# Performance work log

Hardware: AMD Instinct MI355X
Metric: run time of the kernel (lower is better)

Reference implementation:

```python
import jax, jax.numpy as jnp
import numpy as np
from math import sqrt

T_TEMP = 1.0  # softmax temperature (init arg T)
NEG_INF = -1e30  # finite stand-in for -inf; masked probs are exactly 0 after softmax


def setup_inputs() -> dict:
    key = jax.random.key(0)
    kq, kk, kv = jax.random.split(key, 3)
    B, L, H, E = 4, 2048, 16, 64
    queries = jax.random.normal(kq, (B, L, H, E), dtype=jnp.float32)
    keys = jax.random.normal(kk, (B, L, H, E), dtype=jnp.float32)
    values = jax.random.normal(kv, (B, L, H, E), dtype=jnp.float32)
    return {"queries": queries, "keys": keys, "values": values}


def reference(queries, keys, values):
    # queries: [B,L,H,E], keys: [B,S,H,E], values: [B,S,H,D]
    B, L, H, E = queries.shape
    S = keys.shape[1]
    scale = 1.0 / sqrt(E)
    # scores: [B,H,L,S]
    scores = jnp.einsum('blhe,bshe->bhls', queries, keys) * scale
    # causal mask: True above diagonal -> masked out (TriangularCausalMask)
    causal = jnp.triu(jnp.ones((L, S), dtype=bool), k=1)
    scores = jnp.where(causal, NEG_INF, scores)
    A = jax.nn.softmax(scores / T_TEMP, axis=-1)  # dropout p=0 -> identity
    V = jnp.einsum('bhls,bshd->blhd', A, values)
    return V
```

## Files before the change

### kernel.cpp

```cpp
#include <hip/hip_runtime.h>


typedef __attribute__((ext_vector_type(8))) unsigned short u16x8;
typedef __attribute__((ext_vector_type(4))) unsigned short u16x4;
typedef __attribute__((ext_vector_type(8))) __bf16 bf16x8;
typedef __attribute__((ext_vector_type(4))) float f32x4;
typedef __attribute__((ext_vector_type(16))) float f32x16;
typedef __attribute__((ext_vector_type(4))) unsigned int u32x4;

#define LOG2E 1.44269504088896340736f
#define AS1 __attribute__((address_space(1)))
#define AS3 __attribute__((address_space(3)))

static __device__ __forceinline__ unsigned short f32_bf16_rne(float x) {
    unsigned int b = __builtin_bit_cast(unsigned int, x);
    b = (b + 0x7fffu + ((b >> 16) & 1u)) >> 16;
    return (unsigned short)b;
}

static __device__ __forceinline__ unsigned int cvt_pk_bf16(float lo, float hi) {
    unsigned int r;
    asm("v_cvt_pk_bf16_f32 %0, %1, %2" : "=v"(r) : "v"(lo), "v"(hi));
    return r;
}

static __device__ __forceinline__ int swzs(int row) {
    return (row & 6) | ((row >> 3) & 1);
}
static __device__ __forceinline__ int tileIdx(int row, int col) {
    return row * 64 + (((col >> 3) ^ swzs(row)) << 3) + (col & 7);
}

__global__ __launch_bounds__(256) void prep_kernel(
    const float* __restrict__ K, const float* __restrict__ V,
    unsigned short* __restrict__ wsK, unsigned short* __restrict__ wsV)
{
    const int ROW = 1024;
    const int tid = threadIdx.x;
    const int kt  = blockIdx.x;
    const int bh  = blockIdx.y;
    const size_t tileBase = (size_t)(bh >> 4) * 2048 * ROW + (size_t)(bh & 15) * 64
                          + (size_t)(kt * 64) * ROW;
    unsigned short* kimg = wsK + (((size_t)bh * 32 + kt) << 12);
    unsigned short* vimg = wsV + (((size_t)bh * 32 + kt) << 12);

    __shared__ __align__(16) unsigned short ik[4096];
    __shared__ unsigned int sT[64 * 33];

    {
        const int key = tid & 63, ec = tid >> 6;
        const float* kr = K + tileBase + (size_t)key * ROW + ec * 16;
        #pragma unroll
        for (int i = 0; i < 4; ++i) {
            f32x4 v = *(const f32x4*)(kr + 4 * i);
            u16x4 w;
            #pragma unroll
            for (int j = 0; j < 4; ++j) w[j] = f32_bf16_rne(v[j]);
            const int e = ec * 16 + 4 * i;
            *(u16x4*)&ik[(e >> 3) * 512 + key * 8 + (e & 7)] = w;
        }
    }

    {
        const int kp = tid & 31, d0 = (tid >> 5) * 8;
        const float* v0 = V + tileBase + (size_t)(2 * kp) * ROW + d0;
        f32x4 a0 = *(const f32x4*)(v0);
        f32x4 a1 = *(const f32x4*)(v0 + 4);
        f32x4 b0 = *(const f32x4*)(v0 + ROW);
        f32x4 b1 = *(const f32x4*)(v0 + ROW + 4);
        #pragma unroll
        for (int i = 0; i < 4; ++i) {
            sT[(d0 + i) * 33 + kp]     = cvt_pk_bf16(a0[i], b0[i]);
            sT[(d0 + 4 + i) * 33 + kp] = cvt_pk_bf16(a1[i], b1[i]);
        }
    }
    __syncthreads();

    {
        const u32x4* src = (const u32x4*)ik;
        u32x4* dst = (u32x4*)kimg;
        dst[tid]       = src[tid];
        dst[256 + tid] = src[256 + tid];
    }
    {
        u32x4* vd = (u32x4*)vimg;
        u32x4 w0, w1;
        #pragma unroll
        for (int j = 0; j < 4; ++j) {
            const int unit = tid;
            const int kc8 = unit >> 6, dx = unit & 63;
            const int d = dx ^ kc8, kp = kc8 * 4 + j;
            w0[j] = sT[d * 33 + kp];
        }
        #pragma unroll
        for (int j = 0; j < 4; ++j) {
            const int unit = 256 + tid;
            const int kc8 = unit >> 6, dx = unit & 63;
            const int d = dx ^ kc8, kp = kc8 * 4 + j;
            w1[j] = sT[d * 33 + kp];
        }
        vd[tid]       = w0;
        vd[256 + tid] = w1;
    }
}

__global__ __launch_bounds__(256, 4) void fattn2_kernel(
    const float* __restrict__ Q,
    const unsigned short* __restrict__ wsK,
    const unsigned short* __restrict__ wsV,
    float* __restrict__ O)
{
    const int ROW = 1024;

    const int tid  = threadIdx.x;
    const int wave = tid >> 6;
    const int lane = tid & 63;
    const int s    = lane >> 5;
    const int n32  = lane & 31;
    const bool hi32 = (s != 0);
    const int qh = wave & 1;
    const int kh = wave >> 1;

    const int id    = blockIdx.x;
    const int qtile = 31 - (id >> 6);
    const int bh    = id & 63;
    const size_t headBase = (size_t)(bh >> 4) * 2048 * ROW + (size_t)(bh & 15) * 64;
    const int q0 = qtile * 64 + qh * 32;

    __shared__ __align__(16) unsigned short sK[2][4096];
    __shared__ __align__(16) unsigned short sV[2][4096];

    const int kBase = s * 1024 + n32 * 16 + kh * 512;
    int vbB[2];
    #pragma unroll
    for (int c = 0; c < 2; ++c)
        vbB[c] = kh * 4096 + c * 2048 + s * 1024
               + ((n32 ^ (4 * kh + 2 * c + s)) << 4);

    const float c0 = 0.125f * LOG2E;

    bf16x8 qf[4];
    {
        const float* qrow = Q + headBase + (size_t)(q0 + n32) * ROW + s * 8;
        #pragma unroll
        for (int c = 0; c < 4; ++c) {
            f32x4 v0 = *(const f32x4*)(qrow + 16 * c);
            f32x4 v1 = *(const f32x4*)(qrow + 16 * c + 4);
            u32x4 a;
            a[0] = cvt_pk_bf16(v0[0] * c0, v0[1] * c0);
            a[1] = cvt_pk_bf16(v0[2] * c0, v0[3] * c0);
            a[2] = cvt_pk_bf16(v1[0] * c0, v1[1] * c0);
            a[3] = cvt_pk_bf16(v1[2] * c0, v1[3] * c0);
            qf[c] = __builtin_bit_cast(bf16x8, a);
        }
    }

    f32x16 oacc0, oacc1;
    #pragma unroll
    for (int r = 0; r < 16; ++r) { oacc0[r] = 0.f; oacc1[r] = 0.f; }
    float l = 0.f;

    const int nT = qtile + 1;

    #define STAGE(buf, kt_)                                                    \
    do {                                                                       \
        const size_t toff = (((size_t)bh * 32 + (kt_)) << 12);                 \
        const unsigned short* kg = wsK + toff + wave * 1024 + lane * 8;        \
        const unsigned short* vg = wsV + toff + wave * 1024 + lane * 8;        \
        __builtin_amdgcn_global_load_lds((const AS1 unsigned int*)kg,          \
            (AS3 unsigned int*)&sK[buf][wave * 1024], 16, 0, 0);               \
        __builtin_amdgcn_global_load_lds((const AS1 unsigned int*)(kg + 512),  \
            (AS3 unsigned int*)&sK[buf][wave * 1024 + 512], 16, 0, 0);         \
        __builtin_amdgcn_global_load_lds((const AS1 unsigned int*)vg,          \
            (AS3 unsigned int*)&sV[buf][wave * 1024], 16, 0, 0);               \
        __builtin_amdgcn_global_load_lds((const AS1 unsigned int*)(vg + 512),  \
            (AS3 unsigned int*)&sV[buf][wave * 1024 + 512], 16, 0, 0);         \
    } while (0)

    STAGE(0, 0);

    for (int kt = 0; kt < nT; ++kt) {
        const int cur = kt & 1;

        __syncthreads();

        if (kt + 1 < nT) STAGE(cur ^ 1, kt + 1);

        if (kt == qtile && kh > qh) continue;

        const char* kb = (const char*)&sK[cur][0];
        const char* vb = (const char*)&sV[cur][0];

        f32x16 sacc;
        #pragma unroll
        for (int r = 0; r < 16; ++r) sacc[r] = 0.f;
        __builtin_amdgcn_s_setprio(1);
        #pragma unroll
        for (int c = 0; c < 4; ++c) {
            bf16x8 k0 = __builtin_bit_cast(bf16x8,
                *(const u16x8*)(kb + kBase + c * 2048));
            sacc = __builtin_amdgcn_mfma_f32_32x32x16_bf16(k0, qf[c], sacc, 0, 0, 0);
        }
        __builtin_amdgcn_s_setprio(0);

        if (kt == qtile && kh == qh) {
            #pragma unroll
            for (int r = 0; r < 16; ++r) {
                const int k0 = (r & 3) + 8 * (r >> 2) + 4 * s;
                sacc[r] = (k0 > n32) ? -1e30f : sacc[r];
            }
        }

        float la = 0.f;
        #pragma unroll
        for (int r = 0; r < 16; ++r) {
            sacc[r] = __builtin_amdgcn_exp2f(fminf(sacc[r], 80.f));
            la += sacc[r];
        }
        l += la;

        bf16x8 bp[2];
        #define XCHG(pe, cc, DST)                                              \
        do {                                                                   \
            unsigned int P0 = cvt_pk_bf16(pe[8*(cc)+0], pe[8*(cc)+1]);         \
            unsigned int P1 = cvt_pk_bf16(pe[8*(cc)+2], pe[8*(cc)+3]);         \
            unsigned int P2 = cvt_pk_bf16(pe[8*(cc)+4], pe[8*(cc)+5]);         \
            unsigned int P3 = cvt_pk_bf16(pe[8*(cc)+6], pe[8*(cc)+7]);         \
            unsigned int x0 = __shfl_xor(P0, 32, 64);                          \
            unsigned int x1 = __shfl_xor(P1, 32, 64);                          \
            unsigned int x2 = __shfl_xor(P2, 32, 64);                          \
            unsigned int x3 = __shfl_xor(P3, 32, 64);                          \
            u32x4 bw;                                                          \
            bw[0] = hi32 ? x2 : P0;                                            \
            bw[1] = hi32 ? x3 : P1;                                            \
            bw[2] = hi32 ? P2 : x0;                                            \
            bw[3] = hi32 ? P3 : x1;                                            \
            DST = __builtin_bit_cast(bf16x8, bw);                              \
        } while (0)
        XCHG(sacc, 0, bp[0]);
        XCHG(sacc, 1, bp[1]);
        #undef XCHG

        __builtin_amdgcn_s_setprio(1);
        #pragma unroll
        for (int c = 0; c < 2; ++c) {
            bf16x8 v0 = __builtin_bit_cast(bf16x8,
                *(const u16x8*)(vb + vbB[c]));
            bf16x8 v1 = __builtin_bit_cast(bf16x8,
                *(const u16x8*)(vb + vbB[c] + 512));
            oacc0 = __builtin_amdgcn_mfma_f32_32x32x16_bf16(v0, bp[c], oacc0, 0, 0, 0);
            oacc1 = __builtin_amdgcn_mfma_f32_32x32x16_bf16(v1, bp[c], oacc1, 0, 0, 0);
        }
        __builtin_amdgcn_s_setprio(0);
    }
    #undef STAGE

    l += __shfl_xor(l, 32, 64);

    __syncthreads();

    float* lbuf = (float*)&sV[0][0];
    lbuf[wave * 32 + n32] = l;
    float* tb = (float*)&sK[0][0] + qh * 2048;
    if (kh == 1) {
        #pragma unroll
        for (int rr = 0; rr < 4; ++rr) {
            f32x4 w0, w1;
            #pragma unroll
            for (int j = 0; j < 4; ++j) {
                w0[j] = oacc0[4 * rr + j];
                w1[j] = oacc1[4 * rr + j];
            }
            const int s40 = 2 * rr + s;
            const int s41 = 8 + 2 * rr + s;
            *(f32x4*)&tb[n32 * 64 + ((s40 ^ (n32 & 15)) << 2)] = w0;
            *(f32x4*)&tb[n32 * 64 + ((s41 ^ (n32 & 15)) << 2)] = w1;
        }
    }
    __syncthreads();
    if (kh == 0) {
        const float inv = 1.0f / (l + lbuf[64 + qh * 32 + n32]);
        #pragma unroll
        for (int rr = 0; rr < 4; ++rr) {
            const int s40 = 2 * rr + s;
            const int s41 = 8 + 2 * rr + s;
            float* a0 = &tb[n32 * 64 + ((s40 ^ (n32 & 15)) << 2)];
            float* a1 = &tb[n32 * 64 + ((s41 ^ (n32 & 15)) << 2)];
            f32x4 p0 = *(const f32x4*)a0;
            f32x4 p1 = *(const f32x4*)a1;
            #pragma unroll
            for (int j = 0; j < 4; ++j) {
                p0[j] = (p0[j] + oacc0[4 * rr + j]) * inv;
                p1[j] = (p1[j] + oacc1[4 * rr + j]) * inv;
            }
            *(f32x4*)a0 = p0;
            *(f32x4*)a1 = p1;
        }
        #pragma unroll
        for (int it = 0; it < 8; ++it) {
            const int row = (lane >> 2) + 16 * (it & 1);
            const int c4  = (lane & 3) + 4 * (it >> 1);
            f32x4 v = *(const f32x4*)&tb[row * 64 + ((c4 ^ (row & 15)) << 2)];
            *(f32x4*)&O[headBase + (size_t)(q0 + row) * ROW + c4 * 4] = v;
        }
    }
}

__global__ __launch_bounds__(256, 4) void fattn_kernel(
    const float* __restrict__ Q,
    const float* __restrict__ K,
    const float* __restrict__ V,
    float* __restrict__ O)
{
    const int ROW = 1024;
    const int tid  = threadIdx.x;
    const int wave = tid >> 6;
    const int lane = tid & 63;
    const int quad = lane >> 4;
    const int n16  = lane & 15;
    const int xb = blockIdx.x;
    const int bh = blockIdx.y;
    const size_t headBase = (size_t)(bh >> 4) * 2048 * ROW + (size_t)(bh & 15) * 64;

    __shared__ __align__(16) unsigned short sK[4096];
    __shared__ __align__(16) unsigned short sV[4096];
    __shared__ __align__(16) unsigned short sP[4][1024];

    int kvIdx[4];
    #pragma unroll
    for (int nb = 0; nb < 4; ++nb) {
        const int row = nb * 16 + n16;
        kvIdx[nb] = row * 64 + ((quad ^ swzs(row)) << 3);
    }
    const int pIdx = n16 * 64 + ((quad ^ swzs(n16)) << 3);
    const int kStageRow = tid >> 4;
    const int kStageCol = (tid & 15) * 4;
    const int vKey2  = (tid & 31) * 2;
    const int vDbase = (tid >> 5) * 8;
    const float c0 = 0.125f * LOG2E;

    for (int qi = 0; qi < 2; ++qi) {
        const int qtile = qi ? (31 - xb) : xb;
        const int q0 = qtile * 64 + wave * 16;
        bf16x8 qf0, qf1;
        {
            const float* qrow = Q + headBase + (size_t)(q0 + n16) * ROW + quad * 8;
            u16x8 a, b;
            #pragma unroll
            for (int i = 0; i < 8; ++i) {
                a[i] = f32_bf16_rne(qrow[i] * c0);
                b[i] = f32_bf16_rne(qrow[32 + i] * c0);
            }
            qf0 = __builtin_bit_cast(bf16x8, a);
            qf1 = __builtin_bit_cast(bf16x8, b);
        }
        f32x4 oacc[4];
        #pragma unroll
        for (int d = 0; d < 4; ++d) oacc[d] = (f32x4){0.f, 0.f, 0.f, 0.f};
        float l_r[4];
        #pragma unroll
        for (int r = 0; r < 4; ++r) l_r[r] = 0.f;
        const int nT = qtile + 1;
        f32x4 pk[4], pva[2], pvb[2];
        {
            const float* kb = K + headBase;
            const float* r0 = V + headBase + (size_t)vKey2 * ROW + vDbase;
            #pragma unroll
            for (int j = 0; j < 4; ++j)
                pk[j] = *(const f32x4*)(kb + (size_t)(j * 16 + kStageRow) * ROW + kStageCol);
            #pragma unroll
            for (int j = 0; j < 2; ++j) {
                pva[j] = *(const f32x4*)(r0 + j * 4);
                pvb[j] = *(const f32x4*)(r0 + ROW + j * 4);
            }
        }
        for (int kt = 0; kt < nT; ++kt) {
            __syncthreads();
            #pragma unroll
            for (int j = 0; j < 4; ++j) {
                u16x4 w;
                #pragma unroll
                for (int i = 0; i < 4; ++i) w[i] = f32_bf16_rne(pk[j][i]);
                *(u16x4*)&sK[tileIdx(j * 16 + kStageRow, kStageCol)] = w;
            }
            #pragma unroll
            for (int j = 0; j < 2; ++j) {
                const int d0 = vDbase + j * 4;
                #pragma unroll
                for (int i = 0; i < 4; ++i) {
                    unsigned int pkk = (unsigned int)f32_bf16_rne(pva[j][i])
                                     | ((unsigned int)f32_bf16_rne(pvb[j][i]) << 16);
                    *(unsigned int*)&sV[tileIdx(d0 + i, vKey2)] = pkk;
                }
            }
            if (kt + 1 < nT) {
                const size_t nb2 = headBase + (size_t)((kt + 1) * 64) * ROW;
                const float* kb = K + nb2;
                const float* r0 = V + nb2 + (size_t)vKey2 * ROW + vDbase;
                #pragma unroll
                for (int j = 0; j < 4; ++j)
                    pk[j] = *(const f32x4*)(kb + (size_t)(j * 16 + kStageRow) * ROW + kStageCol);
                #pragma unroll
                for (int j = 0; j < 2; ++j) {
                    pva[j] = *(const f32x4*)(r0 + j * 4);
                    pvb[j] = *(const f32x4*)(r0 + ROW + j * 4);
                }
            }
            __syncthreads();
            f32x4 sacc[4];
            #pragma unroll
            for (int nb = 0; nb < 4; ++nb) {
                bf16x8 b0 = __builtin_bit_cast(bf16x8, *(const u16x8*)&sK[kvIdx[nb]]);
                bf16x8 b1 = __builtin_bit_cast(bf16x8, *(const u16x8*)&sK[kvIdx[nb] ^ 32]);
                f32x4 ss = (f32x4){0.f, 0.f, 0.f, 0.f};
                ss = __builtin_amdgcn_mfma_f32_16x16x32_bf16(qf0, b0, ss, 0, 0, 0);
                ss = __builtin_amdgcn_mfma_f32_16x16x32_bf16(qf1, b1, ss, 0, 0, 0);
                sacc[nb] = ss;
            }
            if (kt == qtile) {
                #pragma unroll
                for (int nb = 0; nb < 4; ++nb) {
                    const int keyl = nb * 16 + n16;
                    #pragma unroll
                    for (int r = 0; r < 4; ++r) {
                        const int ql = wave * 16 + quad * 4 + r;
                        sacc[nb][r] = (keyl > ql) ? -1e30f : sacc[nb][r];
                    }
                }
            }
            #pragma unroll
            for (int r = 0; r < 4; ++r) {
                const int qrl = quad * 4 + r;
                const int pwBase = qrl * 64 + (n16 & 7);
                const int sw = swzs(qrl);
                const int hb = n16 >> 3;
                float ps = 0.f;
                #pragma unroll
                for (int nb = 0; nb < 4; ++nb) {
                    unsigned short u = f32_bf16_rne(__builtin_amdgcn_exp2f(sacc[nb][r]));
                    ps += __builtin_bit_cast(float, (unsigned int)u << 16);
                    sP[wave][pwBase + (((nb * 2 + hb) ^ sw) << 3)] = u;
                }
                l_r[r] += ps;
            }
            #pragma unroll
            for (int kh = 0; kh < 2; ++kh) {
                bf16x8 ap = __builtin_bit_cast(bf16x8,
                    *(const u16x8*)&sP[wave][pIdx ^ (kh << 5)]);
                #pragma unroll
                for (int d = 0; d < 4; ++d) {
                    bf16x8 vf = __builtin_bit_cast(bf16x8,
                        *(const u16x8*)&sV[kvIdx[d] ^ (kh << 5)]);
                    oacc[d] = __builtin_amdgcn_mfma_f32_16x16x32_bf16(ap, vf, oacc[d], 0, 0, 0);
                }
            }
        }
        float inv[4];
        #pragma unroll
        for (int r = 0; r < 4; ++r) {
            float l = l_r[r];
            #pragma unroll
            for (int off = 1; off < 16; off <<= 1)
                l += __shfl_xor(l, off, 64);
            inv[r] = 1.0f / l;
        }
        #pragma unroll
        for (int d = 0; d < 4; ++d) {
            #pragma unroll
            for (int r = 0; r < 4; ++r) {
                const int qg = q0 + quad * 4 + r;
                O[headBase + (size_t)qg * ROW + d * 16 + n16] = oacc[d][r] * inv[r];
            }
        }
    }
}

extern "C" void kernel_launch(void* const* d_in, const int* in_sizes, int n_in,
                              void* d_out, int out_size, void* d_ws, size_t ws_size,
                              hipStream_t stream) {
    const float* Q = (const float*)d_in[0];
    const float* K = (const float*)d_in[1];
    const float* V = (const float*)d_in[2];
    float* Out = (float*)d_out;

    const size_t imgElems = (size_t)64 * 32 * 4096;
    if (ws_size >= imgElems * 2 * sizeof(unsigned short)) {
        unsigned short* wsK = (unsigned short*)d_ws;
        unsigned short* wsV = wsK + imgElems;
        hipLaunchKernelGGL(prep_kernel, dim3(32, 64), dim3(256), 0, stream, K, V, wsK, wsV);
        hipLaunchKernelGGL(fattn2_kernel, dim3(2048), dim3(256), 0, stream, Q, wsK, wsV, Out);
    } else {
        hipLaunchKernelGGL(fattn_kernel, dim3(16, 64), dim3(256), 0, stream, Q, K, V, Out);
    }
}
```

Before: 191.3 us.

## Fuse K/V bf16 conversion into attention kernel, dropping separate prep pass

Removes the prep kernel that converted K and V to bf16 tile images in workspace. The attention kernel now loads fp32 K/V tiles directly into registers one tile ahead, converts them to bf16, and writes them into swizzled LDS before each step. This saves one kernel launch and the write and read-back of the workspace images. In exchange, each block re-reads and re-converts fp32 K/V, which doubles global bytes per tile and redoes the conversion many times across query tiles. It also replaces the async global-to-LDS copies with register staging, adding VGPR pressure. The old fallback kernel is deleted.

```diff
diff --git a/kernel.cpp b/kernel.cpp
--- a/kernel.cpp
+++ b/kernel.cpp
@@ -2,21 +2,12 @@
 
 
 typedef __attribute__((ext_vector_type(8))) unsigned short u16x8;
-typedef __attribute__((ext_vector_type(4))) unsigned short u16x4;
 typedef __attribute__((ext_vector_type(8))) __bf16 bf16x8;
 typedef __attribute__((ext_vector_type(4))) float f32x4;
 typedef __attribute__((ext_vector_type(16))) float f32x16;
 typedef __attribute__((ext_vector_type(4))) unsigned int u32x4;
 
 #define LOG2E 1.44269504088896340736f
-#define AS1 __attribute__((address_space(1)))
-#define AS3 __attribute__((address_space(3)))
-
-static __device__ __forceinline__ unsigned short f32_bf16_rne(float x) {
-    unsigned int b = __builtin_bit_cast(unsigned int, x);
-    b = (b + 0x7fffu + ((b >> 16) & 1u)) >> 16;
-    return (unsigned short)b;
-}
 
 static __device__ __forceinline__ unsigned int cvt_pk_bf16(float lo, float hi) {
     unsigned int r;
@@ -24,90 +15,10 @@
     return r;
 }
 
-static __device__ __forceinline__ int swzs(int row) {
-    return (row & 6) | ((row >> 3) & 1);
-}
-static __device__ __forceinline__ int tileIdx(int row, int col) {
-    return row * 64 + (((col >> 3) ^ swzs(row)) << 3) + (col & 7);
-}
-
-__global__ __launch_bounds__(256) void prep_kernel(
-    const float* __restrict__ K, const float* __restrict__ V,
-    unsigned short* __restrict__ wsK, unsigned short* __restrict__ wsV)
-{
-    const int ROW = 1024;
-    const int tid = threadIdx.x;
-    const int kt  = blockIdx.x;
-    const int bh  = blockIdx.y;
-    const size_t tileBase = (size_t)(bh >> 4) * 2048 * ROW + (size_t)(bh & 15) * 64
-                          + (size_t)(kt * 64) * ROW;
-    unsigned short* kimg = wsK + (((size_t)bh * 32 + kt) << 12);
-    unsigned short* vimg = wsV + (((size_t)bh * 32 + kt) << 12);
-
-    __shared__ __align__(16) unsigned short ik[4096];
-    __shared__ unsigned int sT[64 * 33];
-
-    {
-        const int key = tid & 63, ec = tid >> 6;
-        const float* kr = K + tileBase + (size_t)key * ROW + ec * 16;
-        #pragma unroll
-        for (int i = 0; i < 4; ++i) {
-            f32x4 v = *(const f32x4*)(kr + 4 * i);
-            u16x4 w;
-            #pragma unroll
-            for (int j = 0; j < 4; ++j) w[j] = f32_bf16_rne(v[j]);
-            const int e = ec * 16 + 4 * i;
-            *(u16x4*)&ik[(e >> 3) * 512 + key * 8 + (e & 7)] = w;
-        }
-    }
-
-    {
-        const int kp = tid & 31, d0 = (tid >> 5) * 8;
-        const float* v0 = V + tileBase + (size_t)(2 * kp) * ROW + d0;
-        f32x4 a0 = *(const f32x4*)(v0);
-        f32x4 a1 = *(const f32x4*)(v0 + 4);
-        f32x4 b0 = *(const f32x4*)(v0 + ROW);
-        f32x4 b1 = *(const f32x4*)(v0 + ROW + 4);
-        #pragma unroll
-        for (int i = 0; i < 4; ++i) {
-            sT[(d0 + i) * 33 + kp]     = cvt_pk_bf16(a0[i], b0[i]);
-            sT[(d0 + 4 + i) * 33 + kp] = cvt_pk_bf16(a1[i], b1[i]);
-        }
-    }
-    __syncthreads();
-
-    {
-        const u32x4* src = (const u32x4*)ik;
-        u32x4* dst = (u32x4*)kimg;
-        dst[tid]       = src[tid];
-        dst[256 + tid] = src[256 + tid];
-    }
-    {
-        u32x4* vd = (u32x4*)vimg;
-        u32x4 w0, w1;
-        #pragma unroll
-        for (int j = 0; j < 4; ++j) {
-            const int unit = tid;
-            const int kc8 = unit >> 6, dx = unit & 63;
-            const int d = dx ^ kc8, kp = kc8 * 4 + j;
-            w0[j] = sT[d * 33 + kp];
-        }
-        #pragma unroll
-        for (int j = 0; j < 4; ++j) {
-            const int unit = 256 + tid;
-            const int kc8 = unit >> 6, dx = unit & 63;
-            const int d = dx ^ kc8, kp = kc8 * 4 + j;
-            w1[j] = sT[d * 33 + kp];
-        }
-        vd[tid]       = w0;
-        vd[256 + tid] = w1;
-    }
-}
-
-__global__ __launch_bounds__(256, 4) void fattn2_kernel(
+__global__ __launch_bounds__(256, 4) void fattn3_kernel(
     const float* __restrict__ Q,
-    const unsigned short* __restrict__ wsK,
-    const unsigned short* __restrict__ wsV,
+    const float* __restrict__ K,
+    const float* __restrict__ V,
     float* __restrict__ O)
 {
     const int ROW = 1024;
@@ -129,6 +40,13 @@
 
     __shared__ __align__(16) unsigned short sK[2][4096];
     __shared__ __align__(16) unsigned short sV[2][4096];
+
+    const int kKey = tid & 63;
+    const int kEc2 = tid >> 6;
+    const int vKp  = tid & 31;
+    const int vD0  = (tid >> 5) * 8;
+    const int kc8  = vKp >> 2;
+    const int mBase = (kc8 * 64 + vD0) * 4 + (vKp & 3);
 
     const int kBase = s * 1024 + n32 * 16 + kh * 512;
     int vbB[2];
@@ -162,29 +80,54 @@
 
     const int nT = qtile + 1;
 
-    #define STAGE(buf, kt_)                                                    \
+    f32x4 pk4[4], pvA[2], pvB[2];
+    #define PREFETCH(kt_)                                                      \
     do {                                                                       \
-        const size_t toff = (((size_t)bh * 32 + (kt_)) << 12);                 \
-        const unsigned short* kg = wsK + toff + wave * 1024 + lane * 8;        \
-        const unsigned short* vg = wsV + toff + wave * 1024 + lane * 8;        \
-        __builtin_amdgcn_global_load_lds((const AS1 unsigned int*)kg,          \
-            (AS3 unsigned int*)&sK[buf][wave * 1024], 16, 0, 0);               \
-        __builtin_amdgcn_global_load_lds((const AS1 unsigned int*)(kg + 512),  \
-            (AS3 unsigned int*)&sK[buf][wave * 1024 + 512], 16, 0, 0);         \
-        __builtin_amdgcn_global_load_lds((const AS1 unsigned int*)vg,          \
-            (AS3 unsigned int*)&sV[buf][wave * 1024], 16, 0, 0);               \
-        __builtin_amdgcn_global_load_lds((const AS1 unsigned int*)(vg + 512),  \
-            (AS3 unsigned int*)&sV[buf][wave * 1024 + 512], 16, 0, 0);         \
+        const float* kg = K + headBase + (size_t)((kt_) * 64 + kKey) * ROW     \
+                        + kEc2 * 16;                                           \
+        pk4[0] = *(const f32x4*)(kg);                                          \
+        pk4[1] = *(const f32x4*)(kg + 4);                                      \
+        pk4[2] = *(const f32x4*)(kg + 8);                                      \
+        pk4[3] = *(const f32x4*)(kg + 12);                                     \
+        const float* vg = V + headBase + (size_t)((kt_) * 64 + 2 * vKp) * ROW  \
+                        + vD0;                                                 \
+        pvA[0] = *(const f32x4*)(vg);                                          \
+        pvA[1] = *(const f32x4*)(vg + 4);                                      \
+        pvB[0] = *(const f32x4*)(vg + ROW);                                    \
+        pvB[1] = *(const f32x4*)(vg + ROW + 4);                                \
     } while (0)
 
-    STAGE(0, 0);
+    PREFETCH(0);
 
     for (int kt = 0; kt < nT; ++kt) {
         const int cur = kt & 1;
 
+        {
+            u32x4 wa, wb;
+            wa[0] = cvt_pk_bf16(pk4[0][0], pk4[0][1]);
+            wa[1] = cvt_pk_bf16(pk4[0][2], pk4[0][3]);
+            wa[2] = cvt_pk_bf16(pk4[1][0], pk4[1][1]);
+            wa[3] = cvt_pk_bf16(pk4[1][2], pk4[1][3]);
+            wb[0] = cvt_pk_bf16(pk4[2][0], pk4[2][1]);
+            wb[1] = cvt_pk_bf16(pk4[2][2], pk4[2][3]);
+            wb[2] = cvt_pk_bf16(pk4[3][0], pk4[3][1]);
+            wb[3] = cvt_pk_bf16(pk4[3][2], pk4[3][3]);
+            *(u32x4*)&sK[cur][kEc2 * 1024 + kKey * 8]       = wa;
+            *(u32x4*)&sK[cur][kEc2 * 1024 + 512 + kKey * 8] = wb;
+            unsigned int* vdw = (unsigned int*)&sV[cur][0];
+            vdw[mBase + ((0 ^ kc8) << 2)] = cvt_pk_bf16(pvA[0][0], pvB[0][0]);
+            vdw[mBase + ((1 ^ kc8) << 2)] = cvt_pk_bf16(pvA[0][1], pvB[0][1]);
+            vdw[mBase + ((2 ^ kc8) << 2)] = cvt_pk_bf16(pvA[0][2], pvB[0][2]);
+            vdw[mBase + ((3 ^ kc8) << 2)] = cvt_pk_bf16(pvA[0][3], pvB[0][3]);
+            vdw[mBase + ((4 ^ kc8) << 2)] = cvt_pk_bf16(pvA[1][0], pvB[1][0]);
+            vdw[mBase + ((5 ^ kc8) << 2)] = cvt_pk_bf16(pvA[1][1], pvB[1][1]);
+            vdw[mBase + ((6 ^ kc8) << 2)] = cvt_pk_bf16(pvA[1][2], pvB[1][2]);
+            vdw[mBase + ((7 ^ kc8) << 2)] = cvt_pk_bf16(pvA[1][3], pvB[1][3]);
+        }
+
         __syncthreads();
 
-        if (kt + 1 < nT) STAGE(cur ^ 1, kt + 1);
+        if (kt + 1 < nT) PREFETCH(kt + 1);
 
         if (kt == qtile && kh > qh) continue;
 
@@ -253,7 +196,7 @@
         }
         __builtin_amdgcn_s_setprio(0);
     }
-    #undef STAGE
+    #undef PREFETCH
 
     l += __shfl_xor(l, 32, 64);
 
@@ -306,175 +249,6 @@
     }
 }
 
-__global__ __launch_bounds__(256, 4) void fattn_kernel(
-    const float* __restrict__ Q,
-    const float* __restrict__ K,
-    const float* __restrict__ V,
-    float* __restrict__ O)
-{
-    const int ROW = 1024;
-    const int tid  = threadIdx.x;
-    const int wave = tid >> 6;
-    const int lane = tid & 63;
-    const int quad = lane >> 4;
-    const int n16  = lane & 15;
-    const int xb = blockIdx.x;
-    const int bh = blockIdx.y;
-    const size_t headBase = (size_t)(bh >> 4) * 2048 * ROW + (size_t)(bh & 15) * 64;
-
-    __shared__ __align__(16) unsigned short sK[4096];
-    __shared__ __align__(16) unsigned short sV[4096];
-    __shared__ __align__(16) unsigned short sP[4][1024];
-
-    int kvIdx[4];
-    #pragma unroll
-    for (int nb = 0; nb < 4; ++nb) {
-        const int row = nb * 16 + n16;
-        kvIdx[nb] = row * 64 + ((quad ^ swzs(row)) << 3);
-    }
-    const int pIdx = n16 * 64 + ((quad ^ swzs(n16)) << 3);
-    const int kStageRow = tid >> 4;
-    const int kStageCol = (tid & 15) * 4;
-    const int vKey2  = (tid & 31) * 2;
-    const int vDbase = (tid >> 5) * 8;
-    const float c0 = 0.125f * LOG2E;
-
-    for (int qi = 0; qi < 2; ++qi) {
-        const int qtile = qi ? (31 - xb) : xb;
-        const int q0 = qtile * 64 + wave * 16;
-        bf16x8 qf0, qf1;
-        {
-            const float* qrow = Q + headBase + (size_t)(q0 + n16) * ROW + quad * 8;
-            u16x8 a, b;
-            #pragma unroll
-            for (int i = 0; i < 8; ++i) {
-                a[i] = f32_bf16_rne(qrow[i] * c0);
-                b[i] = f32_bf16_rne(qrow[32 + i] * c0);
-            }
-            qf0 = __builtin_bit_cast(bf16x8, a);
-            qf1 = __builtin_bit_cast(bf16x8, b);
-        }
-        f32x4 oacc[4];
-        #pragma unroll
-        for (int d = 0; d < 4; ++d) oacc[d] = (f32x4){0.f, 0.f, 0.f, 0.f};
-        float l_r[4];
-        #pragma unroll
-        for (int r = 0; r < 4; ++r) l_r[r] = 0.f;
-        const int nT = qtile + 1;
-        f32x4 pk[4], pva[2], pvb[2];
-        {
-            const float* kb = K + headBase;
-            const float* r0 = V + headBase + (size_t)vKey2 * ROW + vDbase;
-            #pragma unroll
-            for (int j = 0; j < 4; ++j)
-                pk[j] = *(const f32x4*)(kb + (size_t)(j * 16 + kStageRow) * ROW + kStageCol);
-            #pragma unroll
-            for (int j = 0; j < 2; ++j) {
-                pva[j] = *(const f32x4*)(r0 + j * 4);
-                pvb[j] = *(const f32x4*)(r0 + ROW + j * 4);
-            }
-        }
-        for (int kt = 0; kt < nT; ++kt) {
-            __syncthreads();
-            #pragma unroll
-            for (int j = 0; j < 4; ++j) {
-                u16x4 w;
-                #pragma unroll
-                for (int i = 0; i < 4; ++i) w[i] = f32_bf16_rne(pk[j][i]);
-                *(u16x4*)&sK[tileIdx(j * 16 + kStageRow, kStageCol)] = w;
-            }
-            #pragma unroll
-            for (int j = 0; j < 2; ++j) {
-                const int d0 = vDbase + j * 4;
-                #pragma unroll
-                for (int i = 0; i < 4; ++i) {
-                    unsigned int pkk = (unsigned int)f32_bf16_rne(pva[j][i])
-                                     | ((unsigned int)f32_bf16_rne(pvb[j][i]) << 16);
-                    *(unsigned int*)&sV[tileIdx(d0 + i, vKey2)] = pkk;
-                }
-            }
-            if (kt + 1 < nT) {
-                const size_t nb2 = headBase + (size_t)((kt + 1) * 64) * ROW;
-                const float* kb = K + nb2;
-                const float* r0 = V + nb2 + (size_t)vKey2 * ROW + vDbase;
-                #pragma unroll
-                for (int j = 0; j < 4; ++j)
-                    pk[j] = *(const f32x4*)(kb + (size_t)(j * 16 + kStageRow) * ROW + kStageCol);
-                #pragma unroll
-                for (int j = 0; j < 2; ++j) {
-                    pva[j] = *(const f32x4*)(r0 + j * 4);
-                    pvb[j] = *(const f32x4*)(r0 + ROW + j * 4);
-                }
-            }
-            __syncthreads();
-            f32x4 sacc[4];
-            #pragma unroll
-            for (int nb = 0; nb < 4; ++nb) {
-                bf16x8 b0 = __builtin_bit_cast(bf16x8, *(const u16x8*)&sK[kvIdx[nb]]);
-                bf16x8 b1 = __builtin_bit_cast(bf16x8, *(const u16x8*)&sK[kvIdx[nb] ^ 32]);
-                f32x4 ss = (f32x4){0.f, 0.f, 0.f, 0.f};
-                ss = __builtin_amdgcn_mfma_f32_16x16x32_bf16(qf0, b0, ss, 0, 0, 0);
-                ss = __builtin_amdgcn_mfma_f32_16x16x32_bf16(qf1, b1, ss, 0, 0, 0);
-                sacc[nb] = ss;
-            }
-            if (kt == qtile) {
-                #pragma unroll
-                for (int nb = 0; nb < 4; ++nb) {
-                    const int keyl = nb * 16 + n16;
-                    #pragma unroll
-                    for (int r = 0; r < 4; ++r) {
-                        const int ql = wave * 16 + quad * 4 + r;
-                        sacc[nb][r] = (keyl > ql) ? -1e30f : sacc[nb][r];
-                    }
-                }
-            }
-            #pragma unroll
-            for (int r = 0; r < 4; ++r) {
-                const int qrl = quad * 4 + r;
-                const int pwBase = qrl * 64 + (n16 & 7);
-                const int sw = swzs(qrl);
-                const int hb = n16 >> 3;
-                float ps = 0.f;
-                #pragma unroll
-                for (int nb = 0; nb < 4; ++nb) {
-                    unsigned short u = f32_bf16_rne(__builtin_amdgcn_exp2f(sacc[nb][r]));
-                    ps += __builtin_bit_cast(float, (unsigned int)u << 16);
-                    sP[wave][pwBase + (((nb * 2 + hb) ^ sw) << 3)] = u;
-                }
-                l_r[r] += ps;
-            }
-            #pragma unroll
-            for (int kh = 0; kh < 2; ++kh) {
-                bf16x8 ap = __builtin_bit_cast(bf16x8,
-                    *(const u16x8*)&sP[wave][pIdx ^ (kh << 5)]);
-                #pragma unroll
-                for (int d = 0; d < 4; ++d) {
-                    bf16x8 vf = __builtin_bit_cast(bf16x8,
-                        *(const u16x8*)&sV[kvIdx[d] ^ (kh << 5)]);
-                    oacc[d] = __builtin_amdgcn_mfma_f32_16x16x32_bf16(ap, vf, oacc[d], 0, 0, 0);
-                }
-            }
-        }
-        float inv[4];
-        #pragma unroll
-        for (int r = 0; r < 4; ++r) {
-            float l = l_r[r];
-            #pragma unroll
-            for (int off = 1; off < 16; off <<= 1)
-                l += __shfl_xor(l, off, 64);
-            inv[r] = 1.0f / l;
-        }
-        #pragma unroll
-        for (int d = 0; d < 4; ++d) {
-            #pragma unroll
-            for (int r = 0; r < 4; ++r) {
-                const int qg = q0 + quad * 4 + r;
-                O[headBase + (size_t)qg * ROW + d * 16 + n16] = oacc[d][r] * inv[r];
-            }
-        }
-    }
-}
-
 extern "C" void kernel_launch(void* const* d_in, const int* in_sizes, int n_in,
                               void* d_out, int out_size, void* d_ws, size_t ws_size,
                               hipStream_t stream) {
@@ -482,14 +256,7 @@
     const float* K = (const float*)d_in[1];
     const float* V = (const float*)d_in[2];
     float* Out = (float*)d_out;
-
-    const size_t imgElems = (size_t)64 * 32 * 4096;
-    if (ws_size >= imgElems * 2 * sizeof(unsigned short)) {
-        unsigned short* wsK = (unsigned short*)d_ws;
-        unsigned short* wsV = wsK + imgElems;
-        hipLaunchKernelGGL(prep_kernel, dim3(32, 64), dim3(256), 0, stream, K, V, wsK, wsV);
-        hipLaunchKernelGGL(fattn2_kernel, dim3(2048), dim3(256), 0, stream, Q, wsK, wsV, Out);
-    } else {
-        hipLaunchKernelGGL(fattn_kernel, dim3(16, 64), dim3(256), 0, stream, Q, K, V, Out);
-    }
+    (void)d_ws; (void)ws_size;
+
+    hipLaunchKernelGGL(fattn3_kernel, dim3(2048), dim3(256), 0, stream, Q, K, V, Out);
 }
```

Result: slower. 255.9 us (+33.7%).
